# Optimization experiments

Measured on AMD Instinct MI355X. Metric: run time of the kernel, lower is better.

The kernel has to match this reference:

```python
import jax, jax.numpy as jnp
import numpy as np

V, E, S, B, N, H = 32000, 1024, 1024, 4, 4, 16
DH = E // H
DFF = 4 * E
EPS = 1e-6


def _sinusoidal_pe(max_len, d):
    pos = np.arange(max_len)[:, None].astype(np.float32)
    div = np.power(10000.0, np.arange(0, d, 2).astype(np.float32) / d)
    pe = np.zeros((max_len, d), dtype=np.float32)
    pe[:, 0::2] = np.sin(pos / div)
    pe[:, 1::2] = np.cos(pos / div)
    return jnp.asarray(pe)


def layer_norm(x, g, b):
    mu = jnp.mean(x, axis=-1, keepdims=True)
    var = jnp.var(x, axis=-1, keepdims=True)
    return (x - mu) * jax.lax.rsqrt(var + EPS) * g + b


def setup_inputs() -> dict:
    key = jax.random.key(0)
    ks = iter(jax.random.split(key, 32))
    s = 0.02
    d = {}
    d['tokens'] = jax.random.randint(next(ks), (B, S), 0, V)
    d['emb'] = jax.random.normal(next(ks), (V, E), jnp.float32) * s
    d['pe'] = _sinusoidal_pe(S, E)
    # stacked per-layer params, leading dim N
    for name, shape in [('Wq', (N, E, E)), ('Wk', (N, E, E)), ('Wv', (N, E, E)), ('Wo', (N, E, E)),
                        ('W1', (N, E, DFF)), ('W2', (N, DFF, E))]:
        d[name] = jax.random.normal(next(ks), shape, jnp.float32) * s
    for name, shape in [('bq', (N, E)), ('bk', (N, E)), ('bv', (N, E)), ('bo', (N, E)),
                        ('b1', (N, DFF)), ('b2', (N, E))]:
        d[name] = jnp.zeros(shape, jnp.float32)
    d['ln1_g'] = jnp.ones((N, E)); d['ln1_b'] = jnp.zeros((N, E))
    d['ln2_g'] = jnp.ones((N, E)); d['ln2_b'] = jnp.zeros((N, E))
    d['enc_g'] = jnp.ones((E,)); d['enc_b'] = jnp.zeros((E,))
    d['fin_g'] = jnp.ones((E,)); d['fin_b'] = jnp.zeros((E,))
    d['Wout'] = jax.random.normal(next(ks), (E, V), jnp.float32) * s
    d['bout'] = jnp.zeros((V,), jnp.float32)
    return d


def _mha(x, Wq, bq, Wk, bk, Wv, bv, Wo, bo):
    b, s, _ = x.shape
    q = (x @ Wq + bq).reshape(b, s, H, DH)
    k = (x @ Wk + bk).reshape(b, s, H, DH)
    v = (x @ Wv + bv).reshape(b, s, H, DH)
    scores = jnp.einsum('bqhd,bkhd->bhqk', q, k) / jnp.sqrt(jnp.float32(DH))
    attn = jax.nn.softmax(scores, axis=-1)
    out = jnp.einsum('bhqk,bkhd->bqhd', attn, v).reshape(b, s, E)
    return out @ Wo + bo


def reference(tokens, emb, pe, Wq, bq, Wk, bk, Wv, bv, Wo, bo,
              W1, b1, W2, b2, ln1_g, ln1_b, ln2_g, ln2_b,
              enc_g, enc_b, fin_g, fin_b, Wout, bout):
    x = emb[tokens] + pe[None, :tokens.shape[1]]  # [B,S,E]; dropout = identity (eval)
    for i in range(N):
        # sublayer 0: x + LN(MHA(x))  (source's unusual residual order)
        a = _mha(x, Wq[i], bq[i], Wk[i], bk[i], Wv[i], bv[i], Wo[i], bo[i])
        x = x + layer_norm(a, ln1_g[i], ln1_b[i])
        # sublayer 1: x + LN(FF(x))
        f = jax.nn.relu(x @ W1[i] + b1[i]) @ W2[i] + b2[i]
        x = x + layer_norm(f, ln2_g[i], ln2_b[i])
    x = layer_norm(x, enc_g, enc_b)      # encoder final LN
    x = layer_norm(x, fin_g, fin_b)      # Transformer-level LN
    return x @ Wout + bout               # [B,S,V]
```

## Files before the change

### kernel.cpp

```cpp
#include <hip/hip_runtime.h>
#include <hip/hip_bf16.h>
#include <stdint.h>

#define EDIM 1024
#define DFFDIM 4096
#define NLAYER 4
#define BATCH 4
#define SEQ 1024
#define NHEAD 16
#define DHEAD 64
#define VOCAB 32000
#define MROWS (BATCH*SEQ)
#define QKVLD (3*EDIM)
#define EPSF 1e-6f
#define ALPHA 0.18033688011112043f

typedef float f32x4 __attribute__((ext_vector_type(4)));
typedef short s16x8 __attribute__((ext_vector_type(8)));
typedef __bf16 bf16x8 __attribute__((ext_vector_type(8)));

__device__ inline unsigned short f2bf(float f) {
  union { float f; uint32_t u; } v; v.f = f;
  uint32_t r = v.u + 0x7fffu + ((v.u >> 16) & 1u);
  return (unsigned short)(r >> 16);
}

__device__ __forceinline__ float fexp2(float x) {
  float r; asm("v_exp_f32 %0, %1" : "=v"(r) : "v"(x)); return r;
}
__device__ __forceinline__ uint32_t cvtpk(float lo, float hi) {
  uint32_t r; asm("v_cvt_pk_bf16_f32 %0, %1, %2" : "=v"(r) : "v"(lo), "v"(hi)); return r;
}

__device__ __forceinline__ void gload16(const void* g, void* l) {
  __builtin_amdgcn_global_load_lds(
      (const __attribute__((address_space(1))) void*)g,
      (__attribute__((address_space(3))) void*)l, 16, 0, 0);
}

__global__ __launch_bounds__(256) void embed_kernel(
    const int* __restrict__ tokens, const float* __restrict__ emb,
    const float* __restrict__ pe, float* __restrict__ x,
    unsigned short* __restrict__ xb) {
  const int row = blockIdx.x;
  const int s = row & (SEQ - 1);
  const int tok = tokens[row];
  const int c = threadIdx.x * 4;
  float4 ev = *(const float4*)(emb + (size_t)tok * EDIM + c);
  float4 pv = *(const float4*)(pe + (size_t)s * EDIM + c);
  float4 o;
  o.x = ev.x + pv.x; o.y = ev.y + pv.y; o.z = ev.z + pv.z; o.w = ev.w + pv.w;
  *(float4*)(x + (size_t)row * EDIM + c) = o;
  unsigned short* xr = xb + (size_t)row * EDIM + c;
  xr[0] = f2bf(o.x); xr[1] = f2bf(o.y); xr[2] = f2bf(o.z); xr[3] = f2bf(o.w);
}

__global__ __launch_bounds__(256) void transpose_w(
    const float* __restrict__ src, unsigned short* __restrict__ dst,
    int N, int K, float scale) {
  __shared__ float tl[64][65];
  const int t = threadIdx.x;
  const int k0 = blockIdx.x * 64, n0 = blockIdx.y * 64;
  const int c = (t & 15) * 4, r0 = t >> 4;
  #pragma unroll
  for (int i = 0; i < 4; ++i) {
    const int r = r0 + i * 16;
    float4 v = *(const float4*)(src + (size_t)(k0 + r) * N + n0 + c);
    tl[r][c] = v.x; tl[r][c + 1] = v.y; tl[r][c + 2] = v.z; tl[r][c + 3] = v.w;
  }
  __syncthreads();
  #pragma unroll
  for (int i = 0; i < 4; ++i) {
    const int n = r0 + i * 16;
    uint2 o;
    o.x = (uint32_t)f2bf(tl[c + 0][n] * scale) | ((uint32_t)f2bf(tl[c + 1][n] * scale) << 16);
    o.y = (uint32_t)f2bf(tl[c + 2][n] * scale) | ((uint32_t)f2bf(tl[c + 3][n] * scale) << 16);
    *(uint2*)(dst + (size_t)(n0 + n) * K + k0 + c) = o;
  }
}

__global__ __launch_bounds__(256) void pack_bias(
    const float* __restrict__ bq, const float* __restrict__ bk,
    const float* __restrict__ bv, float* __restrict__ dst) {
  const int idx = blockIdx.x * 256 + threadIdx.x;
  if (idx >= NLAYER * QKVLD) return;
  const int layer = idx / QKVLD, c = idx % QKVLD;
  float v;
  if (c < 1024)      v = bq[layer * 1024 + c] * ALPHA;
  else if (c < 2048) v = bk[layer * 1024 + c - 1024];
  else               v = bv[layer * 1024 + c - 2048];
  dst[idx] = v;
}

template<int BM, int OUT_BF16, int RELU>
__global__ __launch_bounds__(BM * 2, (BM == 256) ? 2 : 3) void gemm3(
    const unsigned short* __restrict__ A, const unsigned short* __restrict__ Bt,
    const float* __restrict__ bias, void* __restrict__ Cout,
    int Nld, int K, int NBLK) {
  constexpr int BUFB = BM * 128;
  constexpr int ABYTES = BM * 64;
  constexpr int WN = (BM == 256) ? 4 : 2;
  constexpr int MF = BM / 32;
  __shared__ __attribute__((aligned(16))) char smb[3 * BUFB];
  const int t = threadIdx.x, lane = t & 63;
  const int wave = t >> 6;
  const int wr = wave / WN, wc = wave % WN;
  const int l15 = lane & 15, lg = lane >> 4;

  const int cpx = gridDim.x >> 3;
  const int bid = blockIdx.x;
  const int swz = (bid & 7) * cpx + (bid >> 3);
  const int m0 = (swz / NBLK) * BM;
  const int n0 = (swz % NBLK) * BM;

  f32x4 acc[MF][4];
  #pragma unroll
  for (int i = 0; i < MF; ++i)
    #pragma unroll
    for (int j = 0; j < 4; ++j)
      acc[i][j] = (f32x4){0.f, 0.f, 0.f, 0.f};

  const int srow = t >> 2;
  const int scol = (((t & 3) ^ ((t >> 3) & 3)) << 3);
  const unsigned short* agp = A  + (size_t)(m0 + srow) * K + scol;
  const unsigned short* bgp = Bt + (size_t)(n0 + srow) * K + scol;
  const size_t rhalf = (size_t)(BM / 2) * K;

  const int cxo = (lg * 16) ^ (((l15 >> 1) & 3) << 4);
  const int rdA = (wr * (BM / 2) + l15) * 64 + cxo;
  const int rdB = ABYTES + (wc * 64 + l15) * 64 + cxo;

  auto stage_tile = [&](int b, int kt) {
    const int k0 = kt * 32;
    char* d = smb + b * BUFB + t * 16;
    gload16(agp + k0, d);
    gload16(agp + rhalf + k0, d + BM * 32);
    gload16(bgp + k0, d + ABYTES);
    gload16(bgp + rhalf + k0, d + ABYTES + BM * 32);
  };

  const int NT = K / 32;
  stage_tile(0, 0);
  stage_tile(1, 1);
  asm volatile("s_waitcnt vmcnt(4)" ::: "memory");
  __builtin_amdgcn_s_barrier();
  __builtin_amdgcn_sched_barrier(0);

  int bufc = 0, bufn = 2;
  for (int tt = 0; tt < NT; ++tt) {
    if (tt + 2 < NT) stage_tile(bufn, tt + 2);

    const char* ab = smb + bufc * BUFB;
    bf16x8 af[MF], bf[4];
    #pragma unroll
    for (int mf = 0; mf < MF; ++mf)
      af[mf] = *(const bf16x8*)(ab + rdA + mf * 1024);
    #pragma unroll
    for (int nf = 0; nf < 4; ++nf)
      bf[nf] = *(const bf16x8*)(ab + rdB + nf * 1024);

    __builtin_amdgcn_s_setprio(1);
    #pragma unroll
    for (int mf = 0; mf < MF; ++mf)
      #pragma unroll
      for (int nf = 0; nf < 4; ++nf)
        acc[mf][nf] = __builtin_amdgcn_mfma_f32_16x16x32_bf16(af[mf], bf[nf], acc[mf][nf], 0, 0, 0);
    __builtin_amdgcn_s_setprio(0);

    if (tt + 2 < NT)      asm volatile("s_waitcnt vmcnt(4)" ::: "memory");
    else if (tt + 1 < NT) asm volatile("s_waitcnt vmcnt(0)" ::: "memory");
    __builtin_amdgcn_sched_barrier(0);
    __builtin_amdgcn_s_barrier();
    __builtin_amdgcn_sched_barrier(0);

    bufc = (bufc == 2) ? 0 : bufc + 1;
    bufn = (bufn == 2) ? 0 : bufn + 1;
  }

  #pragma unroll
  for (int mf = 0; mf < MF; ++mf) {
    #pragma unroll
    for (int nf = 0; nf < 4; ++nf) {
      const int col = n0 + wc * 64 + nf * 16 + l15;
      const float bv = bias[col];
      #pragma unroll
      for (int r = 0; r < 4; ++r) {
        const int row = m0 + wr * (BM / 2) + mf * 16 + lg * 4 + r;
        float val = acc[mf][nf][r] + bv;
        if (RELU) val = fmaxf(val, 0.f);
        if (OUT_BF16)
          ((unsigned short*)Cout)[(size_t)row * Nld + col] = f2bf(val);
        else
          ((float*)Cout)[(size_t)row * Nld + col] = val;
      }
    }
  }
}

__global__ __launch_bounds__(256) void attn_kernel(
    const unsigned short* __restrict__ qkv, unsigned short* __restrict__ ctx) {
  const int b = blockIdx.z, h = blockIdx.y;
  const int t = threadIdx.x, wave = t >> 6, lane = t & 63;
  const int l15 = lane & 15, lg = lane >> 4;
  const int qrow0 = blockIdx.x * 64 + wave * 16;
  const unsigned short* qbs = qkv + (size_t)b * SEQ * QKVLD + h * DHEAD;
  const unsigned short* kbs = qbs + EDIM;
  const unsigned short* vbs = qbs + 2 * EDIM;
  __shared__ unsigned short Ksm[64][72];
  __shared__ unsigned short VTs[64 * 64];
  __shared__ unsigned short p_lds[4][16][72];

  const unsigned short* qp = qbs + (size_t)(qrow0 + l15) * QKVLD + lg * 8;
  bf16x8 a0 = *(const bf16x8*)qp;
  bf16x8 a1 = *(const bf16x8*)(qp + 32);

  f32x4 o0 = {0,0,0,0}, o1 = {0,0,0,0}, o2 = {0,0,0,0}, o3 = {0,0,0,0};
  float m[4], ls[4];
  #pragma unroll
  for (int r = 0; r < 4; ++r) { m[r] = -1e30f; ls[r] = 0.f; }

  const int sr = t >> 2;
  const int sc = (t & 3) * 16;
  const int posw = ((sr & 15) << 2) | (sr >> 4);
  const unsigned short* kgp = kbs + (size_t)sr * QKVLD + sc;
  const unsigned short* vgp = vbs + (size_t)sr * QKVLD + sc;
  const size_t tilestep = (size_t)64 * QKVLD;

  s16x8 kr0 = *(const s16x8*)kgp, kr1 = *(const s16x8*)(kgp + 8);
  s16x8 vr0 = *(const s16x8*)vgp, vr1 = *(const s16x8*)(vgp + 8);

  const int NT = SEQ / 64;
  for (int j = 0; j < NT; ++j) {
    *(s16x8*)&Ksm[sr][sc] = kr0;
    *(s16x8*)&Ksm[sr][sc + 8] = kr1;
    #pragma unroll
    for (int c = 0; c < 2; ++c) {
      s16x8 vv = c ? vr1 : vr0;
      #pragma unroll
      for (int e = 0; e < 8; ++e) {
        const int d = sc + c * 8 + e;
        const int byteo = d * 128 + ((posw * 2) ^ ((d & 7) << 4));
        *(unsigned short*)((char*)VTs + byteo) = (unsigned short)vv[e];
      }
    }
    __syncthreads();

    f32x4 s[4];
    __builtin_amdgcn_s_setprio(1);
    #pragma unroll
    for (int g = 0; g < 4; ++g) {
      bf16x8 k0 = *(const bf16x8*)&Ksm[g * 16 + l15][lg * 8];
      bf16x8 k1 = *(const bf16x8*)&Ksm[g * 16 + l15][32 + lg * 8];
      f32x4 z = {0, 0, 0, 0};
      z = __builtin_amdgcn_mfma_f32_16x16x32_bf16(a0, k0, z, 0, 0, 0);
      s[g] = __builtin_amdgcn_mfma_f32_16x16x32_bf16(a1, k1, z, 0, 0, 0);
    }
    __builtin_amdgcn_s_setprio(0);

    if (j + 1 < NT) {
      const unsigned short* kn = kgp + (size_t)(j + 1) * tilestep;
      const unsigned short* vn = vgp + (size_t)(j + 1) * tilestep;
      kr0 = *(const s16x8*)kn; kr1 = *(const s16x8*)(kn + 8);
      vr0 = *(const s16x8*)vn; vr1 = *(const s16x8*)(vn + 8);
    }

    float mx[4];
    #pragma unroll
    for (int r = 0; r < 4; ++r)
      mx[r] = fmaxf(fmaxf(s[0][r], s[1][r]), fmaxf(s[2][r], s[3][r]));
    #pragma unroll
    for (int off = 1; off < 16; off <<= 1) {
      #pragma unroll
      for (int r = 0; r < 4; ++r) mx[r] = fmaxf(mx[r], __shfl_xor(mx[r], off));
    }

    bool need = false;
    #pragma unroll
    for (int r = 0; r < 4; ++r) need = need || (mx[r] > m[r] + 8.f);
    if (__any(need)) {
      #pragma unroll
      for (int r = 0; r < 4; ++r) {
        const float mn = fmaxf(m[r], mx[r]);
        const float scl = fexp2(m[r] - mn);
        m[r] = mn;
        ls[r] *= scl;
        o0[r] *= scl; o1[r] *= scl; o2[r] *= scl; o3[r] *= scl;
      }
    }
    #pragma unroll
    for (int g = 0; g < 4; ++g)
      #pragma unroll
      for (int r = 0; r < 4; ++r) s[g][r] = fexp2(s[g][r] - m[r]);

    float rs[4];
    #pragma unroll
    for (int r = 0; r < 4; ++r)
      rs[r] = (s[0][r] + s[1][r]) + (s[2][r] + s[3][r]);
    #pragma unroll
    for (int off = 1; off < 16; off <<= 1) {
      #pragma unroll
      for (int r = 0; r < 4; ++r) rs[r] += __shfl_xor(rs[r], off);
    }
    #pragma unroll
    for (int r = 0; r < 4; ++r) {
      ls[r] += rs[r];
      uint2 w;
      w.x = cvtpk(s[0][r], s[1][r]);
      w.y = cvtpk(s[2][r], s[3][r]);
      *(uint2*)((char*)&p_lds[wave][lg * 4 + r][0] + l15 * 8) = w;
    }
    bf16x8 pa0 = *(const bf16x8*)&p_lds[wave][l15][lg * 8];
    bf16x8 pa1 = *(const bf16x8*)&p_lds[wave][l15][32 + lg * 8];

    auto vld = [&](int dg, int c) {
      const int byteo = (dg * 16 + l15) * 128 + ((c * 64 + lg * 16) ^ ((l15 & 7) << 4));
      return *(const bf16x8*)((const char*)VTs + byteo);
    };
    __builtin_amdgcn_s_setprio(1);
    o0 = __builtin_amdgcn_mfma_f32_16x16x32_bf16(pa0, vld(0, 0), o0, 0, 0, 0);
    o1 = __builtin_amdgcn_mfma_f32_16x16x32_bf16(pa0, vld(1, 0), o1, 0, 0, 0);
    o2 = __builtin_amdgcn_mfma_f32_16x16x32_bf16(pa0, vld(2, 0), o2, 0, 0, 0);
    o3 = __builtin_amdgcn_mfma_f32_16x16x32_bf16(pa0, vld(3, 0), o3, 0, 0, 0);
    o0 = __builtin_amdgcn_mfma_f32_16x16x32_bf16(pa1, vld(0, 1), o0, 0, 0, 0);
    o1 = __builtin_amdgcn_mfma_f32_16x16x32_bf16(pa1, vld(1, 1), o1, 0, 0, 0);
    o2 = __builtin_amdgcn_mfma_f32_16x16x32_bf16(pa1, vld(2, 1), o2, 0, 0, 0);
    o3 = __builtin_amdgcn_mfma_f32_16x16x32_bf16(pa1, vld(3, 1), o3, 0, 0, 0);
    __builtin_amdgcn_s_setprio(0);
    __syncthreads();
  }

  unsigned short* cp = ctx + (size_t)b * SEQ * EDIM + h * DHEAD;
  #pragma unroll
  for (int r = 0; r < 4; ++r) {
    unsigned short* cr = cp + (size_t)(qrow0 + lg * 4 + r) * EDIM;
    const float inv = 1.f / ls[r];
    cr[l15]      = f2bf(o0[r] * inv);
    cr[16 + l15] = f2bf(o1[r] * inv);
    cr[32 + l15] = f2bf(o2[r] * inv);
    cr[48 + l15] = f2bf(o3[r] * inv);
  }
}

__global__ __launch_bounds__(256) void ln_add_kernel(
    const float* __restrict__ a, const float* __restrict__ g, const float* __restrict__ bb,
    float* __restrict__ x, unsigned short* __restrict__ xb) {
  const int row = blockIdx.x, t = threadIdx.x;
  const float* ar = a + (size_t)row * EDIM;
  float4 av = *(const float4*)(ar + t * 4);
  float s = av.x + av.y + av.z + av.w;
  float qq = av.x * av.x + av.y * av.y + av.z * av.z + av.w * av.w;
  #pragma unroll
  for (int off = 1; off < 64; off <<= 1) { s += __shfl_xor(s, off); qq += __shfl_xor(qq, off); }
  __shared__ float red[8];
  const int wv = t >> 6;
  if ((t & 63) == 0) { red[wv] = s; red[4 + wv] = qq; }
  __syncthreads();
  s = red[0] + red[1] + red[2] + red[3];
  qq = red[4] + red[5] + red[6] + red[7];
  const float mean = s * (1.f / EDIM);
  const float rstd = rsqrtf(qq * (1.f / EDIM) - mean * mean + EPSF);
  float4 gv = *(const float4*)(g + t * 4);
  float4 bv = *(const float4*)(bb + t * 4);
  float* xr = x + (size_t)row * EDIM;
  float4 xv = *(float4*)(xr + t * 4);
  float4 o;
  o.x = xv.x + (av.x - mean) * rstd * gv.x + bv.x;
  o.y = xv.y + (av.y - mean) * rstd * gv.y + bv.y;
  o.z = xv.z + (av.z - mean) * rstd * gv.z + bv.z;
  o.w = xv.w + (av.w - mean) * rstd * gv.w + bv.w;
  *(float4*)(xr + t * 4) = o;
  unsigned short* xbr = xb + (size_t)row * EDIM + t * 4;
  xbr[0] = f2bf(o.x); xbr[1] = f2bf(o.y); xbr[2] = f2bf(o.z); xbr[3] = f2bf(o.w);
}

__global__ __launch_bounds__(256) void final_ln_kernel(
    const float* __restrict__ x, const float* __restrict__ g1, const float* __restrict__ b1,
    const float* __restrict__ g2, const float* __restrict__ b2,
    unsigned short* __restrict__ xb) {
  const int row = blockIdx.x, t = threadIdx.x;
  __shared__ float red[8];
  const int wv = t >> 6;
  const float* xr = x + (size_t)row * EDIM;
  float4 v = *(const float4*)(xr + t * 4);

  float s = v.x + v.y + v.z + v.w;
  float qq = v.x * v.x + v.y * v.y + v.z * v.z + v.w * v.w;
  #pragma unroll
  for (int off = 1; off < 64; off <<= 1) { s += __shfl_xor(s, off); qq += __shfl_xor(qq, off); }
  if ((t & 63) == 0) { red[wv] = s; red[4 + wv] = qq; }
  __syncthreads();
  s = red[0] + red[1] + red[2] + red[3];
  qq = red[4] + red[5] + red[6] + red[7];
  __syncthreads();
  float mean = s * (1.f / EDIM);
  float rstd = rsqrtf(qq * (1.f / EDIM) - mean * mean + EPSF);
  float4 g1v = *(const float4*)(g1 + t * 4);
  float4 b1v = *(const float4*)(b1 + t * 4);
  float4 tv;
  tv.x = (v.x - mean) * rstd * g1v.x + b1v.x;
  tv.y = (v.y - mean) * rstd * g1v.y + b1v.y;
  tv.z = (v.z - mean) * rstd * g1v.z + b1v.z;
  tv.w = (v.w - mean) * rstd * g1v.w + b1v.w;

  s = tv.x + tv.y + tv.z + tv.w;
  qq = tv.x * tv.x + tv.y * tv.y + tv.z * tv.z + tv.w * tv.w;
  #pragma unroll
  for (int off = 1; off < 64; off <<= 1) { s += __shfl_xor(s, off); qq += __shfl_xor(qq, off); }
  if ((t & 63) == 0) { red[wv] = s; red[4 + wv] = qq; }
  __syncthreads();
  s = red[0] + red[1] + red[2] + red[3];
  qq = red[4] + red[5] + red[6] + red[7];
  mean = s * (1.f / EDIM);
  rstd = rsqrtf(qq * (1.f / EDIM) - mean * mean + EPSF);
  float4 g2v = *(const float4*)(g2 + t * 4);
  float4 b2v = *(const float4*)(b2 + t * 4);
  unsigned short* o = xb + (size_t)row * EDIM + t * 4;
  o[0] = f2bf((tv.x - mean) * rstd * g2v.x + b2v.x);
  o[1] = f2bf((tv.y - mean) * rstd * g2v.y + b2v.y);
  o[2] = f2bf((tv.z - mean) * rstd * g2v.z + b2v.z);
  o[3] = f2bf((tv.w - mean) * rstd * g2v.w + b2v.w);
}

extern "C" void kernel_launch(void* const* d_in, const int* in_sizes, int n_in,
                              void* d_out, int out_size, void* d_ws, size_t ws_size,
                              hipStream_t stream) {
  const int*   tokens = (const int*)d_in[0];
  const float* emb    = (const float*)d_in[1];
  const float* pe     = (const float*)d_in[2];
  const float* Wq     = (const float*)d_in[3];
  const float* Wk     = (const float*)d_in[4];
  const float* Wv     = (const float*)d_in[5];
  const float* Wo     = (const float*)d_in[6];
  const float* W1     = (const float*)d_in[7];
  const float* W2     = (const float*)d_in[8];
  const float* bq     = (const float*)d_in[9];
  const float* bk     = (const float*)d_in[10];
  const float* bv     = (const float*)d_in[11];
  const float* bo     = (const float*)d_in[12];
  const float* b1     = (const float*)d_in[13];
  const float* b2     = (const float*)d_in[14];
  const float* ln1_g  = (const float*)d_in[15];
  const float* ln1_b  = (const float*)d_in[16];
  const float* ln2_g  = (const float*)d_in[17];
  const float* ln2_b  = (const float*)d_in[18];
  const float* enc_g  = (const float*)d_in[19];
  const float* enc_b  = (const float*)d_in[20];
  const float* fin_g  = (const float*)d_in[21];
  const float* fin_b  = (const float*)d_in[22];
  const float* Wout   = (const float*)d_in[23];
  const float* bout   = (const float*)d_in[24];
  float* out = (float*)d_out;

  uint8_t* p = (uint8_t*)d_ws;
  auto alloc = [&](size_t bytes) {
    void* r = (void*)p;
    p += (bytes + 255) & ~(size_t)255;
    return r;
  };
  float*          x     = (float*)alloc((size_t)MROWS * EDIM * 4);
  unsigned short* xb    = (unsigned short*)alloc((size_t)MROWS * EDIM * 2);
  float*          tbuf  = (float*)alloc((size_t)MROWS * EDIM * 4);
  unsigned short* qkv   = (unsigned short*)alloc((size_t)MROWS * QKVLD * 2);
  unsigned short* ctx   = (unsigned short*)alloc((size_t)MROWS * EDIM * 2);
  unsigned short* wlt   = (unsigned short*)alloc((size_t)NLAYER * 12 * 1024 * 1024 * 2);
  unsigned short* woutt = (unsigned short*)alloc((size_t)VOCAB * EDIM * 2);
  float*          bqkv  = (float*)alloc((size_t)NLAYER * QKVLD * 4);
  unsigned short* ff1   = qkv;
  if ((size_t)(p - (uint8_t*)d_ws) > ws_size) return;

  const dim3 blk(256);
  const dim3 blk512(512);
  const size_t LW = (size_t)12 * 1024 * 1024;
  const size_t M1 = 1024 * 1024;

  for (int i = 0; i < NLAYER; ++i) {
    unsigned short* lb = wlt + (size_t)i * LW;
    transpose_w<<<dim3(16, 16),  blk, 0, stream>>>(Wq + (size_t)i * M1, lb,          1024, 1024, ALPHA);
    transpose_w<<<dim3(16, 16),  blk, 0, stream>>>(Wk + (size_t)i * M1, lb + M1,     1024, 1024, 1.0f);
    transpose_w<<<dim3(16, 16),  blk, 0, stream>>>(Wv + (size_t)i * M1, lb + 2 * M1, 1024, 1024, 1.0f);
    transpose_w<<<dim3(16, 16),  blk, 0, stream>>>(Wo + (size_t)i * M1, lb + 3 * M1, 1024, 1024, 1.0f);
    transpose_w<<<dim3(16, 64),  blk, 0, stream>>>(W1 + (size_t)i * 4 * M1, lb + 4 * M1, 4096, 1024, 1.0f);
    transpose_w<<<dim3(64, 16),  blk, 0, stream>>>(W2 + (size_t)i * 4 * M1, lb + 8 * M1, 1024, 4096, 1.0f);
  }
  transpose_w<<<dim3(16, 500), blk, 0, stream>>>(Wout, woutt, VOCAB, 1024, 1.0f);
  pack_bias<<<(NLAYER * QKVLD + 255) / 256, blk, 0, stream>>>(bq, bk, bv, bqkv);

  embed_kernel<<<MROWS, blk, 0, stream>>>(tokens, emb, pe, x, xb);

  const int MB2 = MROWS / 256;
  const int MB1 = MROWS / 128;
  for (int i = 0; i < NLAYER; ++i) {
    unsigned short* lb = wlt + (size_t)i * LW;
    gemm3<256, 1, 0><<<MB2 * (QKVLD / 256), blk512, 0, stream>>>(
        xb, lb, bqkv + (size_t)i * QKVLD, qkv, QKVLD, EDIM, QKVLD / 256);
    attn_kernel<<<dim3(SEQ / 64, NHEAD, BATCH), blk, 0, stream>>>(qkv, ctx);
    gemm3<128, 0, 0><<<MB1 * (EDIM / 128), blk, 0, stream>>>(
        ctx, lb + 3 * M1, bo + i * EDIM, tbuf, EDIM, EDIM, EDIM / 128);
    ln_add_kernel<<<MROWS, blk, 0, stream>>>(tbuf, ln1_g + i * EDIM, ln1_b + i * EDIM, x, xb);
    gemm3<256, 1, 1><<<MB2 * (DFFDIM / 256), blk512, 0, stream>>>(
        xb, lb + 4 * M1, b1 + i * DFFDIM, ff1, DFFDIM, EDIM, DFFDIM / 256);
    gemm3<128, 0, 0><<<MB1 * (EDIM / 128), blk, 0, stream>>>(
        ff1, lb + 8 * M1, b2 + i * EDIM, tbuf, EDIM, DFFDIM, EDIM / 128);
    ln_add_kernel<<<MROWS, blk, 0, stream>>>(tbuf, ln2_g + i * EDIM, ln2_b + i * EDIM, x, xb);
  }

  final_ln_kernel<<<MROWS, blk, 0, stream>>>(x, enc_g, enc_b, fin_g, fin_b, xb);
  gemm3<256, 0, 0><<<MB2 * (VOCAB / 256), blk512, 0, stream>>>(
      xb, woutt, bout, out, VOCAB, EDIM, VOCAB / 256);
}
```

Before: 1.414 ms.

## Add 8-wave double-buffered 256x256 GEMM with phased loads for large GEMMs

Adds a new GEMM kernel that computes a 256x256 tile with 8 waves over a 128KB double-buffered LDS. Each 64-wide k tile is split into four phases, and the global loads for the next tiles are interleaved with MFMA work using explicit waitcnt, barriers and setprio. The kernel replaces the previous BM=256 GEMM for the QKV, FF1 and vocab projections, aiming to hide load latency and raise MFMA utilisation. The 128KB LDS footprint with launch_bounds(512,2) relies on enough LDS per CU for two blocks, and the hand-tuned waitcnt counts are easy to get wrong.

```diff
diff --git a/kernel.cpp b/kernel.cpp
--- a/kernel.cpp
+++ b/kernel.cpp
@@ -90,6 +90,114 @@
   else if (c < 2048) v = bk[layer * 1024 + c - 1024];
   else               v = bv[layer * 1024 + c - 2048];
   dst[idx] = v;
+}
+
+template<int OUT_BF16, int RELU>
+__global__ __launch_bounds__(512, 2) void gemm8k(
+    const unsigned short* __restrict__ A, const unsigned short* __restrict__ Bt,
+    const float* __restrict__ bias, void* __restrict__ Cout,
+    int Nld, int K, int NBLK) {
+  __shared__ __attribute__((aligned(16))) char smb[131072];
+  const int t = threadIdx.x, lane = t & 63;
+  const int wave = t >> 6, wr = wave >> 2, wc = wave & 3;
+  const int l15 = lane & 15, lg = lane >> 4;
+
+  const int cpx = gridDim.x >> 3;
+  const int bid = blockIdx.x;
+  const int swz = (bid & 7) * cpx + (bid >> 3);
+  const int m0 = (swz / NBLK) * 256;
+  const int n0 = (swz % NBLK) * 256;
+
+  f32x4 acc[8][4];
+  #pragma unroll
+  for (int i = 0; i < 8; ++i)
+    #pragma unroll
+    for (int j = 0; j < 4; ++j)
+      acc[i][j] = (f32x4){0.f, 0.f, 0.f, 0.f};
+
+  const int sr_ = t >> 2;
+  const int sc_ = 8 * ((t & 3) ^ ((sr_ >> 1) & 3));
+  const unsigned short* agp = A  + (size_t)(m0 + sr_) * K + sc_;
+  const unsigned short* bgp = Bt + (size_t)(n0 + sr_) * K + sc_;
+  const size_t r128 = (size_t)128 * K;
+
+#define STAGE(db, op, kh, kt) do { \
+    const unsigned short* g_ = ((op) ? bgp : agp) + (size_t)(kt) * 64 + (kh) * 32; \
+    char* d_ = smb + (db) * 65536 + (op) * 32768 + (kh) * 16384 + t * 16; \
+    gload16(g_, d_); gload16(g_ + r128, d_ + 8192); } while (0)
+
+  const int cxo = (lg * 16) ^ (((l15 >> 1) & 3) << 4);
+  const int rdA = (wr * 128 + l15) * 64 + cxo;
+  const int rdB = 32768 + (wc * 64 + l15) * 64 + cxo;
+
+#define PHASE(db, kh, mq, STG, ENDW) do { \
+    bf16x8 a_[4], b_[4]; \
+    const char* rb_ = smb + (db) * 65536 + (kh) * 16384; \
+    _Pragma("unroll") for (int i_ = 0; i_ < 4; ++i_) \
+      a_[i_] = *(const bf16x8*)(rb_ + rdA + ((mq) * 4 + i_) * 1024); \
+    _Pragma("unroll") for (int j_ = 0; j_ < 4; ++j_) \
+      b_[j_] = *(const bf16x8*)(rb_ + rdB + j_ * 1024); \
+    STG; \
+    __builtin_amdgcn_sched_barrier(0); \
+    __builtin_amdgcn_s_barrier(); \
+    asm volatile("s_waitcnt lgkmcnt(0)" ::: "memory"); \
+    __builtin_amdgcn_sched_barrier(0); \
+    __builtin_amdgcn_s_setprio(1); \
+    _Pragma("unroll") for (int i_ = 0; i_ < 4; ++i_) \
+      _Pragma("unroll") for (int j_ = 0; j_ < 4; ++j_) \
+        acc[(mq) * 4 + i_][j_] = __builtin_amdgcn_mfma_f32_16x16x32_bf16( \
+            a_[i_], b_[j_], acc[(mq) * 4 + i_][j_], 0, 0, 0); \
+    __builtin_amdgcn_s_setprio(0); \
+    ENDW; \
+    __builtin_amdgcn_sched_barrier(0); \
+    __builtin_amdgcn_s_barrier(); \
+  } while (0)
+
+#define TILE(db, tt) do { \
+    const bool s1_ = (tt) + 1 < NT, s2_ = (tt) + 2 < NT; \
+    PHASE(db, 0, 0, { if (s1_) STAGE(db ^ 1, 0, 1, (tt) + 1); }, {}); \
+    PHASE(db, 0, 1, { if (s1_) STAGE(db ^ 1, 1, 1, (tt) + 1); }, \
+          { if (s1_) asm volatile("s_waitcnt vmcnt(4)" ::: "memory"); \
+            else     asm volatile("s_waitcnt vmcnt(0)" ::: "memory"); }); \
+    PHASE(db, 1, 0, { if (s2_) STAGE(db, 0, 0, (tt) + 2); }, {}); \
+    PHASE(db, 1, 1, { if (s2_) STAGE(db, 1, 0, (tt) + 2); }, \
+          { asm volatile("s_waitcnt vmcnt(4)" ::: "memory"); }); \
+  } while (0)
+
+  const int NT = K / 64;
+  STAGE(0, 0, 0, 0); STAGE(0, 1, 0, 0);
+  STAGE(0, 0, 1, 0); STAGE(0, 1, 1, 0);
+  STAGE(1, 0, 0, 1); STAGE(1, 1, 0, 1);
+  asm volatile("s_waitcnt vmcnt(8)" ::: "memory");
+  __builtin_amdgcn_s_barrier();
+
+  #pragma unroll 1
+  for (int t2 = 0; t2 < NT; t2 += 2) {
+    TILE(0, t2);
+    TILE(1, t2 + 1);
+  }
+
+  #pragma unroll
+  for (int mf = 0; mf < 8; ++mf) {
+    #pragma unroll
+    for (int nf = 0; nf < 4; ++nf) {
+      const int col = n0 + wc * 64 + nf * 16 + l15;
+      const float bv = bias[col];
+      #pragma unroll
+      for (int r = 0; r < 4; ++r) {
+        const int row = m0 + wr * 128 + mf * 16 + lg * 4 + r;
+        float val = acc[mf][nf][r] + bv;
+        if (RELU) val = fmaxf(val, 0.f);
+        if (OUT_BF16)
+          ((unsigned short*)Cout)[(size_t)row * Nld + col] = f2bf(val);
+        else
+          ((float*)Cout)[(size_t)row * Nld + col] = val;
+      }
+    }
+  }
+#undef TILE
+#undef PHASE
+#undef STAGE
 }
 
 template<int BM, int OUT_BF16, int RELU>
@@ -491,13 +599,13 @@
   const int MB1 = MROWS / 128;
   for (int i = 0; i < NLAYER; ++i) {
     unsigned short* lb = wlt + (size_t)i * LW;
-    gemm3<256, 1, 0><<<MB2 * (QKVLD / 256), blk512, 0, stream>>>(
+    gemm8k<1, 0><<<MB2 * (QKVLD / 256), blk512, 0, stream>>>(
         xb, lb, bqkv + (size_t)i * QKVLD, qkv, QKVLD, EDIM, QKVLD / 256);
     attn_kernel<<<dim3(SEQ / 64, NHEAD, BATCH), blk, 0, stream>>>(qkv, ctx);
     gemm3<128, 0, 0><<<MB1 * (EDIM / 128), blk, 0, stream>>>(
         ctx, lb + 3 * M1, bo + i * EDIM, tbuf, EDIM, EDIM, EDIM / 128);
     ln_add_kernel<<<MROWS, blk, 0, stream>>>(tbuf, ln1_g + i * EDIM, ln1_b + i * EDIM, x, xb);
-    gemm3<256, 1, 1><<<MB2 * (DFFDIM / 256), blk512, 0, stream>>>(
+    gemm8k<1, 1><<<MB2 * (DFFDIM / 256), blk512, 0, stream>>>(
         xb, lb + 4 * M1, b1 + i * DFFDIM, ff1, DFFDIM, EDIM, DFFDIM / 256);
     gemm3<128, 0, 0><<<MB1 * (EDIM / 128), blk, 0, stream>>>(
         ff1, lb + 8 * M1, b2 + i * EDIM, tbuf, EDIM, DFFDIM, EDIM / 128);
@@ -505,6 +613,6 @@
   }
 
   final_ln_kernel<<<MROWS, blk, 0, stream>>>(x, enc_g, enc_b, fin_g, fin_b, xb);
-  gemm3<256, 0, 0><<<MB2 * (VOCAB / 256), blk512, 0, stream>>>(
+  gemm8k<0, 0><<<MB2 * (VOCAB / 256), blk512, 0, stream>>>(
       xb, woutt, bout, out, VOCAB, EDIM, VOCAB / 256);
 }
```

After: 1.431 ms. Within noise of the previous version (+1.2%).

## Transpose attention MFMAs to keep P in registers and drop LDS round-trip

Applied to the files above, without the earlier changes.

Swaps the operand order of both attention MFMAs (S^T = K·Q^T, O^T = V^T·P^T), so each lane holds one query row's scores. The P tile can then be packed to bf16 straight from registers instead of going through a per-wave LDS buffer, and the row max and row sum need only two cross-lane shuffles instead of four-step butterflies over four rows. To match the new K ordering, the V-transpose store permutation in LDS is remapped. The epilogue writes packed 64-bit bf16 stores. Getting the key-position permutation wrong would silently corrupt the output.

```diff
diff --git a/kernel.cpp b/kernel.cpp
--- a/kernel.cpp
+++ b/kernel.cpp
@@ -208,20 +208,19 @@
   const unsigned short* vbs = qbs + 2 * EDIM;
   __shared__ unsigned short Ksm[64][72];
   __shared__ unsigned short VTs[64 * 64];
-  __shared__ unsigned short p_lds[4][16][72];
 
   const unsigned short* qp = qbs + (size_t)(qrow0 + l15) * QKVLD + lg * 8;
   bf16x8 a0 = *(const bf16x8*)qp;
   bf16x8 a1 = *(const bf16x8*)(qp + 32);
 
-  f32x4 o0 = {0,0,0,0}, o1 = {0,0,0,0}, o2 = {0,0,0,0}, o3 = {0,0,0,0};
-  float m[4], ls[4];
-  #pragma unroll
-  for (int r = 0; r < 4; ++r) { m[r] = -1e30f; ls[r] = 0.f; }
+  f32x4 o[4];
+  #pragma unroll
+  for (int dg = 0; dg < 4; ++dg) o[dg] = (f32x4){0.f, 0.f, 0.f, 0.f};
+  float m = -1e30f, ls = 0.f;
 
   const int sr = t >> 2;
   const int sc = (t & 3) * 16;
-  const int posw = ((sr & 15) << 2) | (sr >> 4);
+  const int posw = (((sr >> 4) & 1) << 5) | (((sr & 15) >> 2) << 3) | (((sr >> 5) & 1) << 2) | (sr & 3);
   const unsigned short* kgp = kbs + (size_t)sr * QKVLD + sc;
   const unsigned short* vgp = vbs + (size_t)sr * QKVLD + sc;
   const size_t tilestep = (size_t)64 * QKVLD;
@@ -252,8 +251,8 @@
       bf16x8 k0 = *(const bf16x8*)&Ksm[g * 16 + l15][lg * 8];
       bf16x8 k1 = *(const bf16x8*)&Ksm[g * 16 + l15][32 + lg * 8];
       f32x4 z = {0, 0, 0, 0};
-      z = __builtin_amdgcn_mfma_f32_16x16x32_bf16(a0, k0, z, 0, 0, 0);
-      s[g] = __builtin_amdgcn_mfma_f32_16x16x32_bf16(a1, k1, z, 0, 0, 0);
+      z = __builtin_amdgcn_mfma_f32_16x16x32_bf16(k0, a0, z, 0, 0, 0);
+      s[g] = __builtin_amdgcn_mfma_f32_16x16x32_bf16(k1, a1, z, 0, 0, 0);
     }
     __builtin_amdgcn_s_setprio(0);
 
@@ -264,80 +263,66 @@
       vr0 = *(const s16x8*)vn; vr1 = *(const s16x8*)(vn + 8);
     }
 
-    float mx[4];
-    #pragma unroll
-    for (int r = 0; r < 4; ++r)
-      mx[r] = fmaxf(fmaxf(s[0][r], s[1][r]), fmaxf(s[2][r], s[3][r]));
-    #pragma unroll
-    for (int off = 1; off < 16; off <<= 1) {
-      #pragma unroll
-      for (int r = 0; r < 4; ++r) mx[r] = fmaxf(mx[r], __shfl_xor(mx[r], off));
+    float mx = s[0][0];
+    #pragma unroll
+    for (int g = 0; g < 4; ++g)
+      #pragma unroll
+      for (int r = 0; r < 4; ++r) mx = fmaxf(mx, s[g][r]);
+    mx = fmaxf(mx, __shfl_xor(mx, 16));
+    mx = fmaxf(mx, __shfl_xor(mx, 32));
+
+    if (__any(mx > m + 8.f)) {
+      const float mn = fmaxf(m, mx);
+      const float scl = fexp2(m - mn);
+      m = mn;
+      ls *= scl;
+      #pragma unroll
+      for (int dg = 0; dg < 4; ++dg)
+        #pragma unroll
+        for (int r = 0; r < 4; ++r) o[dg][r] *= scl;
     }
-
-    bool need = false;
-    #pragma unroll
-    for (int r = 0; r < 4; ++r) need = need || (mx[r] > m[r] + 8.f);
-    if (__any(need)) {
-      #pragma unroll
-      for (int r = 0; r < 4; ++r) {
-        const float mn = fmaxf(m[r], mx[r]);
-        const float scl = fexp2(m[r] - mn);
-        m[r] = mn;
-        ls[r] *= scl;
-        o0[r] *= scl; o1[r] *= scl; o2[r] *= scl; o3[r] *= scl;
-      }
-    }
     #pragma unroll
     for (int g = 0; g < 4; ++g)
       #pragma unroll
-      for (int r = 0; r < 4; ++r) s[g][r] = fexp2(s[g][r] - m[r]);
-
-    float rs[4];
-    #pragma unroll
-    for (int r = 0; r < 4; ++r)
-      rs[r] = (s[0][r] + s[1][r]) + (s[2][r] + s[3][r]);
-    #pragma unroll
-    for (int off = 1; off < 16; off <<= 1) {
-      #pragma unroll
-      for (int r = 0; r < 4; ++r) rs[r] += __shfl_xor(rs[r], off);
-    }
-    #pragma unroll
-    for (int r = 0; r < 4; ++r) {
-      ls[r] += rs[r];
-      uint2 w;
-      w.x = cvtpk(s[0][r], s[1][r]);
-      w.y = cvtpk(s[2][r], s[3][r]);
-      *(uint2*)((char*)&p_lds[wave][lg * 4 + r][0] + l15 * 8) = w;
-    }
-    bf16x8 pa0 = *(const bf16x8*)&p_lds[wave][l15][lg * 8];
-    bf16x8 pa1 = *(const bf16x8*)&p_lds[wave][l15][32 + lg * 8];
+      for (int r = 0; r < 4; ++r) s[g][r] = fexp2(s[g][r] - m);
+
+    float rs = 0.f;
+    #pragma unroll
+    for (int g = 0; g < 4; ++g)
+      rs += (s[g][0] + s[g][1]) + (s[g][2] + s[g][3]);
+    rs += __shfl_xor(rs, 16);
+    rs += __shfl_xor(rs, 32);
+    ls += rs;
+
+    union { uint32_t u[4]; bf16x8 v; } pb0, pb1;
+    pb0.u[0] = cvtpk(s[0][0], s[0][1]); pb0.u[1] = cvtpk(s[0][2], s[0][3]);
+    pb0.u[2] = cvtpk(s[2][0], s[2][1]); pb0.u[3] = cvtpk(s[2][2], s[2][3]);
+    pb1.u[0] = cvtpk(s[1][0], s[1][1]); pb1.u[1] = cvtpk(s[1][2], s[1][3]);
+    pb1.u[2] = cvtpk(s[3][0], s[3][1]); pb1.u[3] = cvtpk(s[3][2], s[3][3]);
 
     auto vld = [&](int dg, int c) {
       const int byteo = (dg * 16 + l15) * 128 + ((c * 64 + lg * 16) ^ ((l15 & 7) << 4));
       return *(const bf16x8*)((const char*)VTs + byteo);
     };
     __builtin_amdgcn_s_setprio(1);
-    o0 = __builtin_amdgcn_mfma_f32_16x16x32_bf16(pa0, vld(0, 0), o0, 0, 0, 0);
-    o1 = __builtin_amdgcn_mfma_f32_16x16x32_bf16(pa0, vld(1, 0), o1, 0, 0, 0);
-    o2 = __builtin_amdgcn_mfma_f32_16x16x32_bf16(pa0, vld(2, 0), o2, 0, 0, 0);
-    o3 = __builtin_amdgcn_mfma_f32_16x16x32_bf16(pa0, vld(3, 0), o3, 0, 0, 0);
-    o0 = __builtin_amdgcn_mfma_f32_16x16x32_bf16(pa1, vld(0, 1), o0, 0, 0, 0);
-    o1 = __builtin_amdgcn_mfma_f32_16x16x32_bf16(pa1, vld(1, 1), o1, 0, 0, 0);
-    o2 = __builtin_amdgcn_mfma_f32_16x16x32_bf16(pa1, vld(2, 1), o2, 0, 0, 0);
-    o3 = __builtin_amdgcn_mfma_f32_16x16x32_bf16(pa1, vld(3, 1), o3, 0, 0, 0);
+    #pragma unroll
+    for (int dg = 0; dg < 4; ++dg)
+      o[dg] = __builtin_amdgcn_mfma_f32_16x16x32_bf16(vld(dg, 0), pb0.v, o[dg], 0, 0, 0);
+    #pragma unroll
+    for (int dg = 0; dg < 4; ++dg)
+      o[dg] = __builtin_amdgcn_mfma_f32_16x16x32_bf16(vld(dg, 1), pb1.v, o[dg], 0, 0, 0);
     __builtin_amdgcn_s_setprio(0);
     __syncthreads();
   }
 
-  unsigned short* cp = ctx + (size_t)b * SEQ * EDIM + h * DHEAD;
-  #pragma unroll
-  for (int r = 0; r < 4; ++r) {
-    unsigned short* cr = cp + (size_t)(qrow0 + lg * 4 + r) * EDIM;
-    const float inv = 1.f / ls[r];
-    cr[l15]      = f2bf(o0[r] * inv);
-    cr[16 + l15] = f2bf(o1[r] * inv);
-    cr[32 + l15] = f2bf(o2[r] * inv);
-    cr[48 + l15] = f2bf(o3[r] * inv);
+  unsigned short* cp = ctx + (size_t)b * SEQ * EDIM + h * DHEAD + (size_t)(qrow0 + l15) * EDIM;
+  const float inv = 1.f / ls;
+  #pragma unroll
+  for (int dg = 0; dg < 4; ++dg) {
+    uint2 w;
+    w.x = cvtpk(o[dg][0] * inv, o[dg][1] * inv);
+    w.y = cvtpk(o[dg][2] * inv, o[dg][3] * inv);
+    *(uint2*)(cp + dg * 16 + lg * 4) = w;
   }
 }
 
```

Measured after the change: 1.340 ms. 1.06x faster.
